# Kernel optimization log

Hardware: AMD Instinct MI355X
Metric: run time of the kernel (lower is better)

Reference implementation:

```python
import jax, jax.numpy as jnp
import numpy as np

DIM = 320
HEADS = 8
D_HEAD = 40
CTX_DIM = 768
INNER_FF = 4 * DIM  # 1280
EPS = 1e-5


def _ln(x, w, b):
    mu = jnp.mean(x, axis=-1, keepdims=True)
    var = jnp.mean(jnp.square(x - mu), axis=-1, keepdims=True)
    return (x - mu) * jax.lax.rsqrt(var + EPS) * w + b


def _attn(xq, ctx, Wq, Wk, Wv, Wo, bo):
    # Wq: [dim, inner]; Wk/Wv: [ctx_dim, inner]; Wo: [inner, dim]
    b, n, _ = xq.shape
    m = ctx.shape[1]
    scale = D_HEAD ** -0.5
    q = (xq @ Wq).reshape(b, n, HEADS, D_HEAD)
    k = (ctx @ Wk).reshape(b, m, HEADS, D_HEAD)
    v = (ctx @ Wv).reshape(b, m, HEADS, D_HEAD)
    sim = jnp.einsum('bihd,bjhd->bhij', q, k) * scale
    attn = jax.nn.softmax(sim, axis=-1)
    out = jnp.einsum('bhij,bjhd->bihd', attn, v).reshape(b, n, HEADS * D_HEAD)
    return out @ Wo + bo


def setup_inputs() -> dict:
    key = jax.random.key(0)
    ks = jax.random.split(key, 20)
    s = 0.02
    inner = HEADS * D_HEAD  # 320
    d = {
        'x': jax.random.normal(ks[0], (2, 4096, DIM), jnp.float32),
        'context': jax.random.normal(ks[1], (2, 77, CTX_DIM), jnp.float32),
        # norm params
        'ln1_w': jnp.ones((DIM,)), 'ln1_b': jnp.zeros((DIM,)),
        'ln2_w': jnp.ones((DIM,)), 'ln2_b': jnp.zeros((DIM,)),
        'ln3_w': jnp.ones((DIM,)), 'ln3_b': jnp.zeros((DIM,)),
        # attn1 (self)
        'a1_Wq': jax.random.normal(ks[2], (DIM, inner)) * s,
        'a1_Wk': jax.random.normal(ks[3], (DIM, inner)) * s,
        'a1_Wv': jax.random.normal(ks[4], (DIM, inner)) * s,
        'a1_Wo': jax.random.normal(ks[5], (inner, DIM)) * s,
        'a1_bo': jnp.zeros((DIM,)),
        # attn2 (cross)
        'a2_Wq': jax.random.normal(ks[6], (DIM, inner)) * s,
        'a2_Wk': jax.random.normal(ks[7], (CTX_DIM, inner)) * s,
        'a2_Wv': jax.random.normal(ks[8], (CTX_DIM, inner)) * s,
        'a2_Wo': jax.random.normal(ks[9], (inner, DIM)) * s,
        'a2_bo': jnp.zeros((DIM,)),
        # GEGLU feed-forward
        'ff_W1': jax.random.normal(ks[10], (DIM, 2 * INNER_FF)) * s,
        'ff_b1': jnp.zeros((2 * INNER_FF,)),
        'ff_W2': jax.random.normal(ks[11], (INNER_FF, DIM)) * s,
        'ff_b2': jnp.zeros((DIM,)),
    }
    return d


def reference(x, context, ln1_w, ln1_b, ln2_w, ln2_b, ln3_w, ln3_b,
              a1_Wq, a1_Wk, a1_Wv, a1_Wo, a1_bo,
              a2_Wq, a2_Wk, a2_Wv, a2_Wo, a2_bo,
              ff_W1, ff_b1, ff_W2, ff_b2):
    h = _ln(x, ln1_w, ln1_b)
    x = _attn(h, h, a1_Wq, a1_Wk, a1_Wv, a1_Wo, a1_bo) + x
    h = _ln(x, ln2_w, ln2_b)
    x = _attn(h, context, a2_Wq, a2_Wk, a2_Wv, a2_Wo, a2_bo) + x
    h = _ln(x, ln3_w, ln3_b)
    proj = h @ ff_W1 + ff_b1
    u, gate = jnp.split(proj, 2, axis=-1)
    ff = (u * jax.nn.gelu(gate, approximate=False)) @ ff_W2 + ff_b2
    return ff + x
```

## Files before the change

kernel.cpp:

```cpp
#include <hip/hip_runtime.h>
#include <hip/hip_bf16.h>
#include <math.h>

typedef __hip_bfloat16 bf16;
typedef __attribute__((ext_vector_type(8))) short bf16x8;
typedef __attribute__((ext_vector_type(4))) short bf16x4;
typedef __attribute__((ext_vector_type(4))) float f32x4;
typedef __attribute__((ext_vector_type(2))) unsigned int u32x2;

#define DIM 320
#define HEADS 8
#define DHEAD 40
#define CTXD 768
#define FFI 1280
#define NQ 4096
#define NCTX 77
#define BATCH 2

static __device__ __forceinline__ short f2bs(float v) {
    union { bf16 b; short s; } x; x.b = __float2bfloat16(v); return x.s;
}
static __device__ __forceinline__ float bs2f(short s) {
    return __uint_as_float(((unsigned)(unsigned short)s) << 16);
}
static __device__ __forceinline__ unsigned pkbf(float hi, float lo) {
    return __builtin_amdgcn_perm(__float_as_uint(hi), __float_as_uint(lo), 0x07060302u);
}

__global__ void __launch_bounds__(256) prep_kernel(
    const float* q1s, const float* k1s, const float* v1s, const float* o1s,
    const float* q2s, const float* o2s, const float* k2s, const float* v2s,
    const float* w1s, const float* w2s,
    short* q1d, short* k1d, short* v1d, short* o1d,
    short* q2d, short* o2d, short* k2d, short* v2d,
    short* w1d, short* w2d,
    const float* x, const float* ln1w, const float* ln1b, short* h)
{
    int bid = blockIdx.x;
    if (bid < 2280) {
        const float* W; short* Wt; int K, N, base;
        if (bid < 600) {
            int ws = bid / 100; base = bid % 100; K = DIM; N = DIM;
            W  = ws == 0 ? q1s : ws == 1 ? k1s : ws == 2 ? v1s : ws == 3 ? o1s : ws == 4 ? q2s : o2s;
            Wt = ws == 0 ? q1d : ws == 1 ? k1d : ws == 2 ? v1d : ws == 3 ? o1d : ws == 4 ? q2d : o2d;
        } else if (bid < 1080) {
            int i = bid - 600; int ws = i / 240; base = i % 240; K = CTXD; N = DIM;
            W = ws ? v2s : k2s; Wt = ws ? v2d : k2d;
        } else if (bid < 1880) {
            base = bid - 1080; K = DIM; N = 2 * FFI; W = w1s; Wt = w1d;
        } else {
            base = bid - 1880; K = FFI; N = DIM; W = w2s; Wt = w2d;
        }
        int ntx = N / 32;
        int n0 = (base % ntx) * 32, k0 = (base / ntx) * 32;
        __shared__ float T[32][33];
        int c = threadIdx.x & 31, r8 = threadIdx.x >> 5;
#pragma unroll
        for (int rr = 0; rr < 4; ++rr) {
            int r = r8 + rr * 8;
            T[r][c] = W[(size_t)(k0 + r) * N + n0 + c];
        }
        __syncthreads();
#pragma unroll
        for (int rr = 0; rr < 4; ++rr) {
            int r = r8 + rr * 8;
            Wt[(size_t)(n0 + r) * K + k0 + c] = f2bs(T[c][r]);
        }
    } else {
        int row = (bid - 2280) * 4 + (threadIdx.x >> 6);
        int lane = threadIdx.x & 63;
        float v[8];
        float s = 0.f, s2 = 0.f;
        if (lane < 40) {
            const float* rp = x + (size_t)row * DIM + lane * 8;
#pragma unroll
            for (int j = 0; j < 8; ++j) { v[j] = rp[j]; s += v[j]; s2 += v[j] * v[j]; }
        }
#pragma unroll
        for (int off = 32; off; off >>= 1) { s += __shfl_xor(s, off); s2 += __shfl_xor(s2, off); }
        float mean = s * (1.f / DIM);
        float var = s2 * (1.f / DIM) - mean * mean;
        float rstd = rsqrtf(var + 1e-5f);
        if (lane < 40) {
            bf16x8 ov;
#pragma unroll
            for (int j = 0; j < 8; ++j)
                ov[j] = f2bs((v[j] - mean) * rstd * ln1w[lane * 8 + j] + ln1b[lane * 8 + j]);
            *(bf16x8*)(h + (size_t)row * DIM + lane * 8) = ov;
        }
    }
}

__global__ void __launch_bounds__(256) ln_b16(const short* __restrict__ srcp,
                          const float* __restrict__ w, const float* __restrict__ bp,
                          short* __restrict__ out)
{
    int row = blockIdx.x * 4 + (threadIdx.x >> 6);
    int lane = threadIdx.x & 63;
    float v[8];
    float s = 0.f, s2 = 0.f;
    if (lane < 40) {
        bf16x8 xv = *(const bf16x8*)(srcp + (size_t)row * DIM + lane * 8);
#pragma unroll
        for (int j = 0; j < 8; ++j) { v[j] = bs2f(xv[j]); s += v[j]; s2 += v[j] * v[j]; }
    }
#pragma unroll
    for (int off = 32; off; off >>= 1) { s += __shfl_xor(s, off); s2 += __shfl_xor(s2, off); }
    float mean = s * (1.f / DIM);
    float var = s2 * (1.f / DIM) - mean * mean;
    float rstd = rsqrtf(var + 1e-5f);
    if (lane < 40) {
        bf16x8 ov;
#pragma unroll
        for (int j = 0; j < 8; ++j)
            ov[j] = f2bs((v[j] - mean) * rstd * w[lane * 8 + j] + bp[lane * 8 + j]);
        *(bf16x8*)(out + (size_t)row * DIM + lane * 8) = ov;
    }
}

template<int MODE>
__global__ void __launch_bounds__(256) gemm128(const short* __restrict__ A,
                          const short* __restrict__ Wt,
                          const float* __restrict__ bias,
                          const float* __restrict__ res,
                          short* __restrict__ resb,
                          short* __restrict__ outb,
                          float* __restrict__ outf,
                          int N, int K, float oscale)
{
    __shared__ short As[128 * 72];
    __shared__ short Bs[64 * 72];
    const int tid = threadIdx.x;
    const int w = tid >> 6, lane = tid & 63, lrow = lane & 15, lgrp = lane >> 4;
    const int wr = w >> 1, wc = w & 1;
    const int m0 = blockIdx.y * 128, n0 = blockIdx.x * 64;
    f32x4 acc[4][2] = {};
    for (int k0 = 0; k0 < K; k0 += 64) {
        __syncthreads();
#pragma unroll
        for (int l = 0; l < 4; ++l) {
            int idx = tid + (l << 8);
            int arow = idx >> 3, ac = idx & 7;
            *(bf16x8*)&As[arow * 72 + ac * 8] =
                *(const bf16x8*)(A + (size_t)(m0 + arow) * K + k0 + ac * 8);
        }
#pragma unroll
        for (int l = 0; l < 2; ++l) {
            int idx = tid + (l << 8);
            int brow = idx >> 3, bc = idx & 7;
            *(bf16x8*)&Bs[brow * 72 + bc * 8] =
                *(const bf16x8*)(Wt + (size_t)(n0 + brow) * K + k0 + bc * 8);
        }
        __syncthreads();
#pragma unroll
        for (int s = 0; s < 2; ++s) {
            bf16x8 b0 = *(const bf16x8*)&Bs[(wc * 32 + lrow) * 72 + s * 32 + lgrp * 8];
            bf16x8 b1 = *(const bf16x8*)&Bs[(wc * 32 + 16 + lrow) * 72 + s * 32 + lgrp * 8];
#pragma unroll
            for (int m = 0; m < 4; ++m) {
                bf16x8 a = *(const bf16x8*)&As[(wr * 64 + m * 16 + lrow) * 72 + s * 32 + lgrp * 8];
                acc[m][0] = __builtin_amdgcn_mfma_f32_16x16x32_bf16(a, b0, acc[m][0], 0, 0, 0);
                acc[m][1] = __builtin_amdgcn_mfma_f32_16x16x32_bf16(a, b1, acc[m][1], 0, 0, 0);
            }
        }
    }
#pragma unroll
    for (int n = 0; n < 2; ++n) {
        int col = n0 + wc * 32 + n * 16 + lrow;
        float bvx = bias ? bias[col] : 0.f;
#pragma unroll
        for (int m = 0; m < 4; ++m) {
#pragma unroll
            for (int r = 0; r < 4; ++r) {
                int row = m0 + wr * 64 + m * 16 + lgrp * 4 + r;
                float v = acc[m][n][r] + bvx;
                size_t o = (size_t)row * N + col;
                if (MODE == 0)      outb[o] = f2bs(v * oscale);
                else if (MODE == 1) resb[o] = f2bs(v + res[o]);
                else if (MODE == 2) resb[o] = f2bs(v + bs2f(resb[o]));
                else                outf[o] = v + bs2f(resb[o]);
            }
        }
    }
}

__global__ void __launch_bounds__(256) qkv128(const short* __restrict__ A,
                          const short* __restrict__ wq, const short* __restrict__ wk,
                          const short* __restrict__ wv,
                          short* __restrict__ qb, short* __restrict__ kbuf,
                          short* __restrict__ vts, float qscale)
{
    __shared__ short As[128 * 72];
    __shared__ short Bs[64 * 72];
    const int tid = threadIdx.x;
    const int z = blockIdx.z;
    const short* Wt = z == 0 ? wq : z == 1 ? wk : wv;
    const int w = tid >> 6, lane = tid & 63, lrow = lane & 15, lgrp = lane >> 4;
    const int wr = w >> 1, wc = w & 1;
    const int m0 = blockIdx.y * 128, n0 = blockIdx.x * 64;
    f32x4 acc[4][2] = {};
    for (int k0 = 0; k0 < DIM; k0 += 64) {
        __syncthreads();
#pragma unroll
        for (int l = 0; l < 4; ++l) {
            int idx = tid + (l << 8);
            int arow = idx >> 3, ac = idx & 7;
            *(bf16x8*)&As[arow * 72 + ac * 8] =
                *(const bf16x8*)(A + (size_t)(m0 + arow) * DIM + k0 + ac * 8);
        }
#pragma unroll
        for (int l = 0; l < 2; ++l) {
            int idx = tid + (l << 8);
            int brow = idx >> 3, bc = idx & 7;
            *(bf16x8*)&Bs[brow * 72 + bc * 8] =
                *(const bf16x8*)(Wt + (size_t)(n0 + brow) * DIM + k0 + bc * 8);
        }
        __syncthreads();
#pragma unroll
        for (int s = 0; s < 2; ++s) {
            bf16x8 b0 = *(const bf16x8*)&Bs[(wc * 32 + lrow) * 72 + s * 32 + lgrp * 8];
            bf16x8 b1 = *(const bf16x8*)&Bs[(wc * 32 + 16 + lrow) * 72 + s * 32 + lgrp * 8];
#pragma unroll
            for (int m = 0; m < 4; ++m) {
                bf16x8 a = *(const bf16x8*)&As[(wr * 64 + m * 16 + lrow) * 72 + s * 32 + lgrp * 8];
                acc[m][0] = __builtin_amdgcn_mfma_f32_16x16x32_bf16(a, b0, acc[m][0], 0, 0, 0);
                acc[m][1] = __builtin_amdgcn_mfma_f32_16x16x32_bf16(a, b1, acc[m][1], 0, 0, 0);
            }
        }
    }
#pragma unroll
    for (int n = 0; n < 2; ++n) {
        int col = n0 + wc * 32 + n * 16 + lrow;
#pragma unroll
        for (int m = 0; m < 4; ++m) {
            if (z == 2) {
                int row0 = m0 + wr * 64 + m * 16 + lgrp * 4;
                int b_ = row0 >> 12, kv = row0 & (NQ - 1);
                int hh = col / DHEAD, d = col - hh * DHEAD;
                bf16x4 pv;
#pragma unroll
                for (int r = 0; r < 4; ++r) pv[r] = f2bs(acc[m][n][r]);
                *(bf16x4*)(vts + (size_t)((b_ * HEADS + hh) * 48 + d) * NQ + kv) = pv;
            } else {
#pragma unroll
                for (int r = 0; r < 4; ++r) {
                    int row = m0 + wr * 64 + m * 16 + lgrp * 4 + r;
                    float v = acc[m][n][r];
                    if (z == 0) qb[(size_t)row * DIM + col] = f2bs(v * qscale);
                    else        kbuf[(size_t)row * DIM + col] = f2bs(v);
                }
            }
        }
    }
}

__global__ void __launch_bounds__(256) crossq_kv(const short* __restrict__ h,
                          const short* __restrict__ wq2,
                          const float* __restrict__ ctx,
                          const short* __restrict__ wk2, const short* __restrict__ wv2,
                          short* __restrict__ qb, short* __restrict__ k2,
                          short* __restrict__ vt2, float qscale)
{
    __shared__ short As[128 * 72];
    __shared__ short Bs[64 * 72];
    const int tid = threadIdx.x;
    const int w = tid >> 6, lane = tid & 63, lrow = lane & 15, lgrp = lane >> 4;
    int bid = blockIdx.x;
    if (bid < 320) {
        const int wr = w >> 1, wc = w & 1;
        const int m0 = (bid / 5) * 128, n0 = (bid % 5) * 64;
        f32x4 acc[4][2] = {};
        for (int k0 = 0; k0 < DIM; k0 += 64) {
            __syncthreads();
#pragma unroll
            for (int l = 0; l < 4; ++l) {
                int idx = tid + (l << 8);
                int arow = idx >> 3, ac = idx & 7;
                *(bf16x8*)&As[arow * 72 + ac * 8] =
                    *(const bf16x8*)(h + (size_t)(m0 + arow) * DIM + k0 + ac * 8);
            }
#pragma unroll
            for (int l = 0; l < 2; ++l) {
                int idx = tid + (l << 8);
                int brow = idx >> 3, bc = idx & 7;
                *(bf16x8*)&Bs[brow * 72 + bc * 8] =
                    *(const bf16x8*)(wq2 + (size_t)(n0 + brow) * DIM + k0 + bc * 8);
            }
            __syncthreads();
#pragma unroll
            for (int s = 0; s < 2; ++s) {
                bf16x8 b0 = *(const bf16x8*)&Bs[(wc * 32 + lrow) * 72 + s * 32 + lgrp * 8];
                bf16x8 b1 = *(const bf16x8*)&Bs[(wc * 32 + 16 + lrow) * 72 + s * 32 + lgrp * 8];
#pragma unroll
                for (int m = 0; m < 4; ++m) {
                    bf16x8 a = *(const bf16x8*)&As[(wr * 64 + m * 16 + lrow) * 72 + s * 32 + lgrp * 8];
                    acc[m][0] = __builtin_amdgcn_mfma_f32_16x16x32_bf16(a, b0, acc[m][0], 0, 0, 0);
                    acc[m][1] = __builtin_amdgcn_mfma_f32_16x16x32_bf16(a, b1, acc[m][1], 0, 0, 0);
                }
            }
        }
#pragma unroll
        for (int n = 0; n < 2; ++n) {
            int col = n0 + wc * 32 + n * 16 + lrow;
#pragma unroll
            for (int m = 0; m < 4; ++m)
#pragma unroll
                for (int r = 0; r < 4; ++r) {
                    int row = m0 + wr * 64 + m * 16 + lgrp * 4 + r;
                    qb[(size_t)row * DIM + col] = f2bs(acc[m][n][r] * qscale);
                }
        }
    } else {
        int i = bid - 320;
        int z = i / 15, r_ = i % 15;
        const short* Wt = z ? wv2 : wk2;
        const int Mc = BATCH * NCTX;
        const int m0 = (r_ / 5) * 64, n0 = (r_ % 5) * 64;
        f32x4 acc[4] = {};
        for (int kb = 0; kb < CTXD / 64; ++kb) {
            const int k0 = kb << 6;
            __syncthreads();
#pragma unroll
            for (int l = 0; l < 2; ++l) {
                int idx = tid + (l << 8);
                int arow = idx >> 3, ac = idx & 7;
                int grow = m0 + arow;
                bf16x8 v = {};
                if (grow < Mc) {
                    const float* Af = ctx + (size_t)grow * CTXD + k0 + ac * 8;
#pragma unroll
                    for (int j = 0; j < 8; ++j) v[j] = f2bs(Af[j]);
                }
                *(bf16x8*)&As[arow * 72 + ac * 8] = v;
                *(bf16x8*)&Bs[arow * 72 + ac * 8] =
                    *(const bf16x8*)(Wt + (size_t)(n0 + arow) * CTXD + k0 + ac * 8);
            }
            __syncthreads();
#pragma unroll
            for (int s = 0; s < 2; ++s) {
                bf16x8 a = *(const bf16x8*)&As[(w * 16 + lrow) * 72 + s * 32 + lgrp * 8];
#pragma unroll
                for (int ct = 0; ct < 4; ++ct) {
                    bf16x8 b = *(const bf16x8*)&Bs[(ct * 16 + lrow) * 72 + s * 32 + lgrp * 8];
                    acc[ct] = __builtin_amdgcn_mfma_f32_16x16x32_bf16(a, b, acc[ct], 0, 0, 0);
                }
            }
        }
#pragma unroll
        for (int ct = 0; ct < 4; ++ct) {
            int col = n0 + ct * 16 + lrow;
            int hh = col / DHEAD, d = col - hh * DHEAD;
#pragma unroll
            for (int r = 0; r < 4; ++r) {
                int row = m0 + w * 16 + lgrp * 4 + r;
                if (row >= Mc) continue;
                float v = acc[ct][r];
                if (z == 0) k2[(size_t)row * DIM + col] = f2bs(v);
                else {
                    int b_ = row / NCTX, kv = row - b_ * NCTX;
                    vt2[(size_t)((b_ * HEADS + hh) * 48 + d) * 128 + kv] = f2bs(v);
                }
            }
        }
    }
}

__global__ void __launch_bounds__(256) geglu128(const short* __restrict__ A,
                           const short* __restrict__ Wt1,
                           const float* __restrict__ b1, short* __restrict__ G)
{
    __shared__ short As[128 * 72];
    __shared__ short Bu[64 * 72];
    __shared__ short Bg[64 * 72];
    const int tid = threadIdx.x;
    const int w = tid >> 6, lane = tid & 63, lrow = lane & 15, lgrp = lane >> 4;
    const int wr = w >> 1, wc = w & 1;
    const int m0 = blockIdx.y * 128, n0 = blockIdx.x * 64;
    f32x4 au[4][2] = {}, ag[4][2] = {};
    for (int k0 = 0; k0 < DIM; k0 += 64) {
        __syncthreads();
#pragma unroll
        for (int l = 0; l < 4; ++l) {
            int idx = tid + (l << 8);
            int arow = idx >> 3, ac = idx & 7;
            *(bf16x8*)&As[arow * 72 + ac * 8] =
                *(const bf16x8*)(A + (size_t)(m0 + arow) * DIM + k0 + ac * 8);
        }
#pragma unroll
        for (int l = 0; l < 2; ++l) {
            int idx = tid + (l << 8);
            int brow = idx >> 3, bc = idx & 7;
            *(bf16x8*)&Bu[brow * 72 + bc * 8] =
                *(const bf16x8*)(Wt1 + (size_t)(n0 + brow) * DIM + k0 + bc * 8);
            *(bf16x8*)&Bg[brow * 72 + bc * 8] =
                *(const bf16x8*)(Wt1 + (size_t)(FFI + n0 + brow) * DIM + k0 + bc * 8);
        }
        __syncthreads();
#pragma unroll
        for (int s = 0; s < 2; ++s) {
            bf16x8 bu0 = *(const bf16x8*)&Bu[(wc * 32 + lrow) * 72 + s * 32 + lgrp * 8];
            bf16x8 bu1 = *(const bf16x8*)&Bu[(wc * 32 + 16 + lrow) * 72 + s * 32 + lgrp * 8];
            bf16x8 bg0 = *(const bf16x8*)&Bg[(wc * 32 + lrow) * 72 + s * 32 + lgrp * 8];
            bf16x8 bg1 = *(const bf16x8*)&Bg[(wc * 32 + 16 + lrow) * 72 + s * 32 + lgrp * 8];
#pragma unroll
            for (int m = 0; m < 4; ++m) {
                bf16x8 a = *(const bf16x8*)&As[(wr * 64 + m * 16 + lrow) * 72 + s * 32 + lgrp * 8];
                au[m][0] = __builtin_amdgcn_mfma_f32_16x16x32_bf16(a, bu0, au[m][0], 0, 0, 0);
                au[m][1] = __builtin_amdgcn_mfma_f32_16x16x32_bf16(a, bu1, au[m][1], 0, 0, 0);
                ag[m][0] = __builtin_amdgcn_mfma_f32_16x16x32_bf16(a, bg0, ag[m][0], 0, 0, 0);
                ag[m][1] = __builtin_amdgcn_mfma_f32_16x16x32_bf16(a, bg1, ag[m][1], 0, 0, 0);
            }
        }
    }
#pragma unroll
    for (int n = 0; n < 2; ++n) {
        int col = n0 + wc * 32 + n * 16 + lrow;
        float bu = b1[col], bg = b1[FFI + col];
#pragma unroll
        for (int m = 0; m < 4; ++m) {
#pragma unroll
            for (int r = 0; r < 4; ++r) {
                int row = m0 + wr * 64 + m * 16 + lgrp * 4 + r;
                float u = au[m][n][r] + bu;
                float g = ag[m][n][r] + bg;
                float gelu = 0.5f * g * (1.f + erff(g * 0.70710678f));
                G[(size_t)row * FFI + col] = f2bs(u * gelu);
            }
        }
    }
}

template<bool FULL>
__global__ void __launch_bounds__(256) flash_mfma(const short* __restrict__ Q,
                           const short* __restrict__ Kb,
                           const short* __restrict__ VtG,
                           short* __restrict__ O,
                           int kvlen, int kvs)
{
    __shared__ short Ks[2][64 * 64];
    __shared__ short Vt[3][48 * 64];
    __shared__ short Ps[128 * 64];
    const int tid = threadIdx.x;
    const int w = tid >> 6, lane = tid & 63, lrow = lane & 15, lgrp = lane >> 4;
    const int hh = blockIdx.y, b = blockIdx.z;
    const int q0 = blockIdx.x * 128;
    const int swz = (lrow & 7) << 4;

    for (int i = tid; i < 1024; i += 256) ((bf16x8*)Ks)[i] = (bf16x8){};
    for (int i = tid; i < 1152; i += 256) {
        short fill = (((i % 384) >> 3) == 40) ? (short)0x3F80 : (short)0;
        bf16x8 f8 = {fill, fill, fill, fill, fill, fill, fill, fill};
        ((bf16x8*)Vt)[i] = f8;
    }

    const size_t qra = (size_t)(b * NQ + q0 + w * 32 + lrow) * DIM + hh * DHEAD;
    const size_t qrb = qra + (size_t)16 * DIM;
    bf16x8 bq0a = *(const bf16x8*)(Q + qra + lgrp * 8);
    bf16x8 bq0b = *(const bf16x8*)(Q + qrb + lgrp * 8);
    bf16x8 bq1a = {}, bq1b = {};
    if (lgrp == 0) {
        bq1a = *(const bf16x8*)(Q + qra + 32);
        bq1b = *(const bf16x8*)(Q + qrb + 32);
    }

    const int kv0 = tid / 5, cc0 = tid % 5;
    const bool isK1 = tid < 64;
    const int kv1 = (256 + tid) / 5, cc1 = (256 + tid) % 5;
    const int vd1 = (tid - 64) >> 3, vcc1 = (tid - 64) & 7;
    const bool hasV2 = tid < 128;
    const int vd2 = (192 + tid) >> 3, vcc2 = (192 + tid) & 7;

    const size_t kbase = (size_t)b * kvlen;
    const size_t vbase = (size_t)((b * HEADS + hh) * 48);

    const short* kp0 = Kb + (kbase + kv0) * DIM + hh * DHEAD + cc0 * 8;
    const short* kp1 = Kb + (kbase + (isK1 ? kv1 : 0)) * DIM + hh * DHEAD + (isK1 ? cc1 : 0) * 8;
    const short* vp1 = VtG + (vbase + (isK1 ? 0 : vd1)) * kvs + (isK1 ? 0 : vcc1) * 8;
    const short* vp2 = VtG + (vbase + (hasV2 ? vd2 : 0)) * kvs + (hasV2 ? vcc2 : 0) * 8;

    const int koff0 = kv0 * 128 + ((cc0 * 16) ^ ((kv0 & 7) << 4));
    const int koff1 = kv1 * 128 + ((cc1 * 16) ^ ((kv1 & 7) << 4));
    const int voff1 = vd1 * 128 + ((vcc1 * 16) ^ ((vd1 & 7) << 4));
    const int voff2 = vd2 * 128 + ((vcc2 * 16) ^ ((vd2 & 7) << 4));

    bf16x8 st0, st1, st2;
    auto issue = [&]() {
        st0 = *(const bf16x8*)kp0; kp0 += 64 * DIM;
        if (isK1) { st1 = *(const bf16x8*)kp1; kp1 += 64 * DIM; }
        else      { st1 = *(const bf16x8*)vp1; vp1 += 64; }
        if (hasV2) { st2 = *(const bf16x8*)vp2; vp2 += 64; }
    };
    auto commit = [&](char* kb_, char* vb_) {
        *(bf16x8*)(kb_ + koff0) = st0;
        if (isK1)  *(bf16x8*)(kb_ + koff1) = st1;
        else       *(bf16x8*)(vb_ + voff1) = st1;
        if (hasV2) *(bf16x8*)(vb_ + voff2) = st2;
    };

    f32x4 oa[3] = {}, ob[3] = {};

    char* kcur = (char*)Ks[0];
    char* knxt = (char*)Ks[1];
    char* vprev = (char*)Vt[2];
    char* vcur  = (char*)Vt[0];
    char* vnxt  = (char*)Vt[1];
    char* pp = (char*)Ps + (w * 32 + lrow) * 128;

    auto pv_step = [&](char* vb_) {
        __builtin_amdgcn_s_setprio(1);
#pragma unroll
        for (int s = 0; s < 2; ++s) {
            bf16x8 bpa = *(const bf16x8*)(pp + ((s * 64 + lgrp * 16) ^ swz));
            bf16x8 bpb = *(const bf16x8*)(pp + 2048 + ((s * 64 + lgrp * 16) ^ swz));
#pragma unroll
            for (int dt = 0; dt < 3; ++dt) {
                bf16x8 av = *(const bf16x8*)(vb_ + (dt * 16 + lrow) * 128 + ((s * 64 + lgrp * 16) ^ swz));
                oa[dt] = __builtin_amdgcn_mfma_f32_16x16x32_bf16(av, bpa, oa[dt], 0, 0, 0);
                ob[dt] = __builtin_amdgcn_mfma_f32_16x16x32_bf16(av, bpb, ob[dt], 0, 0, 0);
            }
        }
        __builtin_amdgcn_s_setprio(0);
    };

    issue();
    __syncthreads();
    commit(kcur, vcur);
    issue();

    const int ntiles = (kvlen + 63) >> 6;
    for (int t = 0; t < ntiles; ++t) {
        __syncthreads();
        commit(knxt, vnxt);
        issue();

        if (t > 0) pv_step(vprev);

        f32x4 sa[4] = {}, sb[4] = {};
        __builtin_amdgcn_s_setprio(1);
#pragma unroll
        for (int ct = 0; ct < 4; ++ct) {
            const char* krow = kcur + (ct * 16 + lrow) * 128;
            bf16x8 ak0 = *(const bf16x8*)(krow + ((lgrp * 16) ^ swz));
            bf16x8 ak1 = *(const bf16x8*)(krow + ((64 + lgrp * 16) ^ swz));
            sa[ct] = __builtin_amdgcn_mfma_f32_16x16x32_bf16(ak0, bq0a, sa[ct], 0, 0, 0);
            sb[ct] = __builtin_amdgcn_mfma_f32_16x16x32_bf16(ak0, bq0b, sb[ct], 0, 0, 0);
            sa[ct] = __builtin_amdgcn_mfma_f32_16x16x32_bf16(ak1, bq1a, sa[ct], 0, 0, 0);
            sb[ct] = __builtin_amdgcn_mfma_f32_16x16x32_bf16(ak1, bq1b, sb[ct], 0, 0, 0);
        }
        __builtin_amdgcn_s_setprio(0);
        if (!FULL && (t << 6) + 64 > kvlen) {
#pragma unroll
            for (int ct = 0; ct < 4; ++ct)
#pragma unroll
                for (int r = 0; r < 4; ++r)
                    if ((t << 6) + ct * 16 + lgrp * 4 + r >= kvlen) { sa[ct][r] = -1e30f; sb[ct][r] = -1e30f; }
        }
#pragma unroll
        for (int ct = 0; ct < 4; ++ct) {
            float a0 = __builtin_amdgcn_exp2f(sa[ct][0]);
            float a1 = __builtin_amdgcn_exp2f(sa[ct][1]);
            float a2 = __builtin_amdgcn_exp2f(sa[ct][2]);
            float a3 = __builtin_amdgcn_exp2f(sa[ct][3]);
            u32x2 pka; pka[0] = pkbf(a1, a0); pka[1] = pkbf(a3, a2);
            *(u32x2*)(pp + ((ct * 32 + lgrp * 8) ^ swz)) = pka;
            float b0 = __builtin_amdgcn_exp2f(sb[ct][0]);
            float b1 = __builtin_amdgcn_exp2f(sb[ct][1]);
            float b2 = __builtin_amdgcn_exp2f(sb[ct][2]);
            float b3 = __builtin_amdgcn_exp2f(sb[ct][3]);
            u32x2 pkb; pkb[0] = pkbf(b1, b0); pkb[1] = pkbf(b3, b2);
            *(u32x2*)(pp + 2048 + ((ct * 32 + lgrp * 8) ^ swz)) = pkb;
        }
        { char* tk = kcur; kcur = knxt; knxt = tk; }
        { char* tv = vprev; vprev = vcur; vcur = vnxt; vnxt = tv; }
    }
    pv_step(vprev);

    float la = __shfl(oa[2][0], 32 + lrow);
    float lb = __shfl(ob[2][0], 32 + lrow);
    float ia = 1.f / la, ib = 1.f / lb;
#pragma unroll
    for (int dt = 0; dt < 3; ++dt) {
        int dbase = dt * 16 + lgrp * 4;
        if (dbase < DHEAD) {
            u32x2 ova, ovb;
            ova[0] = pkbf(oa[dt][1] * ia, oa[dt][0] * ia);
            ova[1] = pkbf(oa[dt][3] * ia, oa[dt][2] * ia);
            *(u32x2*)(O + qra + dbase) = ova;
            ovb[0] = pkbf(ob[dt][1] * ib, ob[dt][0] * ib);
            ovb[1] = pkbf(ob[dt][3] * ib, ob[dt][2] * ib);
            *(u32x2*)(O + qrb + dbase) = ovb;
        }
    }
}

extern "C" void kernel_launch(void* const* d_in, const int* in_sizes, int n_in,
                              void* d_out, int out_size, void* d_ws, size_t ws_size,
                              hipStream_t stream)
{
    const float* x      = (const float*)d_in[0];
    const float* ctx    = (const float*)d_in[1];
    const float* ln1_w  = (const float*)d_in[2];
    const float* ln1_b  = (const float*)d_in[3];
    const float* ln2_w  = (const float*)d_in[4];
    const float* ln2_b  = (const float*)d_in[5];
    const float* ln3_w  = (const float*)d_in[6];
    const float* ln3_b  = (const float*)d_in[7];
    const float* a1_Wq  = (const float*)d_in[8];
    const float* a1_Wk  = (const float*)d_in[9];
    const float* a1_Wv  = (const float*)d_in[10];
    const float* a1_Wo  = (const float*)d_in[11];
    const float* a1_bo  = (const float*)d_in[12];
    const float* a2_Wq  = (const float*)d_in[13];
    const float* a2_Wk  = (const float*)d_in[14];
    const float* a2_Wv  = (const float*)d_in[15];
    const float* a2_Wo  = (const float*)d_in[16];
    const float* a2_bo  = (const float*)d_in[17];
    const float* ff_W1  = (const float*)d_in[18];
    const float* ff_b1  = (const float*)d_in[19];
    const float* ff_W2  = (const float*)d_in[20];
    const float* ff_b2  = (const float*)d_in[21];

    const int M = BATCH * NQ;
    const float qscale2 = (float)(0.15811388300841898 * 1.4426950408889634);

    char* p = (char*)d_ws;
    auto carve = [&](size_t bytes) { char* r = p; p += (bytes + 255) & ~255ULL; return r; };
    short* h       = (short*)carve((size_t)M * DIM * 2);
    short* qb      = (short*)carve((size_t)M * DIM * 2);
    short* kbuf    = (short*)carve((size_t)M * DIM * 2);
    short* attnout = (short*)carve((size_t)M * DIM * 2);
    short* resb    = (short*)carve((size_t)M * DIM * 2);
    short* gbuf    = (short*)carve((size_t)M * FFI * 2);
    short* VtS     = (short*)carve((size_t)BATCH * HEADS * 48 * NQ * 2);
    short* Vt2     = (short*)carve((size_t)BATCH * HEADS * 48 * 128 * 2);
    short* k2      = (short*)carve((size_t)512 * DIM * 2);
    short* wtq1    = (short*)carve((size_t)DIM * DIM * 2);
    short* wtk1    = (short*)carve((size_t)DIM * DIM * 2);
    short* wtv1    = (short*)carve((size_t)DIM * DIM * 2);
    short* wto1    = (short*)carve((size_t)DIM * DIM * 2);
    short* wtq2    = (short*)carve((size_t)DIM * DIM * 2);
    short* wto2    = (short*)carve((size_t)DIM * DIM * 2);
    short* wtk2    = (short*)carve((size_t)DIM * CTXD * 2);
    short* wtv2    = (short*)carve((size_t)DIM * CTXD * 2);
    short* wt1     = (short*)carve((size_t)2 * FFI * DIM * 2);
    short* wt2     = (short*)carve((size_t)DIM * FFI * 2);

    dim3 blk(256);
    dim3 g128(DIM / 64, M / 128);
    dim3 gattn(NQ / 128, HEADS, BATCH);

    prep_kernel<<<2280 + M / 4, blk, 0, stream>>>(
        a1_Wq, a1_Wk, a1_Wv, a1_Wo, a2_Wq, a2_Wo, a2_Wk, a2_Wv, ff_W1, ff_W2,
        wtq1, wtk1, wtv1, wto1, wtq2, wto2, wtk2, wtv2, wt1, wt2,
        x, ln1_w, ln1_b, h);
    qkv128<<<dim3(5, 64, 3), blk, 0, stream>>>(h, wtq1, wtk1, wtv1, qb, kbuf, VtS, qscale2);
    flash_mfma<true><<<gattn, blk, 0, stream>>>(qb, kbuf, VtS, attnout, NQ, NQ);
    gemm128<1><<<g128, blk, 0, stream>>>(attnout, wto1, a1_bo, x, resb, nullptr, nullptr, DIM, DIM, 1.f);
    ln_b16<<<M / 4, blk, 0, stream>>>(resb, ln2_w, ln2_b, h);
    crossq_kv<<<350, blk, 0, stream>>>(h, wtq2, ctx, wtk2, wtv2, qb, k2, Vt2, qscale2);
    flash_mfma<false><<<gattn, blk, 0, stream>>>(qb, k2, Vt2, attnout, NCTX, 128);
    gemm128<2><<<g128, blk, 0, stream>>>(attnout, wto2, a2_bo, nullptr, resb, nullptr, nullptr, DIM, DIM, 1.f);
    ln_b16<<<M / 4, blk, 0, stream>>>(resb, ln3_w, ln3_b, h);
    geglu128<<<dim3(FFI / 64, M / 128), blk, 0, stream>>>(h, wt1, ff_b1, gbuf);
    gemm128<3><<<g128, blk, 0, stream>>>(gbuf, wt2, ff_b2, nullptr, resb, nullptr, (float*)d_out, DIM, FFI, 1.f);
}
```

Baseline: 221.1 us.

## Split self-attention KV range in two and merge partial outputs

The self-attention flash kernel now splits the 4096-key range into two halves. This doubles the grid to 1024 blocks so the GPU's CUs get more concurrent work and better latency hiding. Each half writes unnormalized bf16 partial outputs plus its row sums, and a new combine kernel adds the two partials and normalizes. In exchange it adds an extra launch, extra global traffic for the partial buffers, and a slight precision risk from storing unnormalized sums in bf16. The merge is only valid because the kernel appears to use no per-split running max.

```diff
diff --git a/kernel.cpp b/kernel.cpp
--- a/kernel.cpp
+++ b/kernel.cpp
@@ -118,6 +118,26 @@
     }
 }
 
+__global__ void __launch_bounds__(256) combine_attn(const short* __restrict__ Opart,
+                          const float* __restrict__ lp, short* __restrict__ out)
+{
+    int row = blockIdx.x * 4 + (threadIdx.x >> 6);
+    int lane = threadIdx.x & 63;
+    if (lane >= 40) return;
+    int c = lane * 8;
+    int hh = c / DHEAD;
+    int b_ = row >> 12, q = row & (NQ - 1);
+    float l = lp[((size_t)(0 * 2 + b_) * HEADS + hh) * NQ + q]
+            + lp[((size_t)(1 * 2 + b_) * HEADS + hh) * NQ + q];
+    float inv = 1.f / l;
+    bf16x8 o1 = *(const bf16x8*)(Opart + (size_t)row * DIM + c);
+    bf16x8 o2 = *(const bf16x8*)(Opart + (size_t)(BATCH * NQ) * DIM + (size_t)row * DIM + c);
+    bf16x8 ov;
+#pragma unroll
+    for (int j = 0; j < 8; ++j) ov[j] = f2bs((bs2f(o1[j]) + bs2f(o2[j])) * inv);
+    *(bf16x8*)(out + (size_t)row * DIM + c) = ov;
+}
+
 template<int MODE>
 __global__ void __launch_bounds__(256) gemm128(const short* __restrict__ A,
                           const short* __restrict__ Wt,
@@ -430,19 +450,24 @@
     }
 }
 
-template<bool FULL>
+template<bool SPLIT>
 __global__ void __launch_bounds__(256) flash_mfma(const short* __restrict__ Q,
                            const short* __restrict__ Kb,
                            const short* __restrict__ VtG,
                            short* __restrict__ O,
-                           int kvlen, int kvs)
+                           float* __restrict__ lp,
+                           int kvlen, int kvs, int ntiles)
 {
     __shared__ short Ks[2][64 * 64];
     __shared__ short Vt[3][48 * 64];
     __shared__ short Ps[128 * 64];
     const int tid = threadIdx.x;
     const int w = tid >> 6, lane = tid & 63, lrow = lane & 15, lgrp = lane >> 4;
-    const int hh = blockIdx.y, b = blockIdx.z;
+    const int hh = blockIdx.y;
+    const int zb = blockIdx.z;
+    const int b = SPLIT ? (zb >> 1) : zb;
+    const int hf = SPLIT ? (zb & 1) : 0;
+    const int kvoff = hf * 2048;
     const int q0 = blockIdx.x * 128;
     const int swz = (lrow & 7) << 4;
 
@@ -470,13 +495,13 @@
     const bool hasV2 = tid < 128;
     const int vd2 = (192 + tid) >> 3, vcc2 = (192 + tid) & 7;
 
-    const size_t kbase = (size_t)b * kvlen;
+    const size_t kbase = (size_t)b * kvlen + kvoff;
     const size_t vbase = (size_t)((b * HEADS + hh) * 48);
 
     const short* kp0 = Kb + (kbase + kv0) * DIM + hh * DHEAD + cc0 * 8;
     const short* kp1 = Kb + (kbase + (isK1 ? kv1 : 0)) * DIM + hh * DHEAD + (isK1 ? cc1 : 0) * 8;
-    const short* vp1 = VtG + (vbase + (isK1 ? 0 : vd1)) * kvs + (isK1 ? 0 : vcc1) * 8;
-    const short* vp2 = VtG + (vbase + (hasV2 ? vd2 : 0)) * kvs + (hasV2 ? vcc2 : 0) * 8;
+    const short* vp1 = VtG + (vbase + (isK1 ? 0 : vd1)) * kvs + kvoff + (isK1 ? 0 : vcc1) * 8;
+    const short* vp2 = VtG + (vbase + (hasV2 ? vd2 : 0)) * kvs + kvoff + (hasV2 ? vcc2 : 0) * 8;
 
     const int koff0 = kv0 * 128 + ((cc0 * 16) ^ ((kv0 & 7) << 4));
     const int koff1 = kv1 * 128 + ((cc1 * 16) ^ ((kv1 & 7) << 4));
@@ -527,7 +552,6 @@
     commit(kcur, vcur);
     issue();
 
-    const int ntiles = (kvlen + 63) >> 6;
     for (int t = 0; t < ntiles; ++t) {
         __syncthreads();
         commit(knxt, vnxt);
@@ -548,7 +572,7 @@
             sb[ct] = __builtin_amdgcn_mfma_f32_16x16x32_bf16(ak1, bq1b, sb[ct], 0, 0, 0);
         }
         __builtin_amdgcn_s_setprio(0);
-        if (!FULL && (t << 6) + 64 > kvlen) {
+        if (!SPLIT && (t << 6) + 64 > kvlen) {
 #pragma unroll
             for (int ct = 0; ct < 4; ++ct)
 #pragma unroll
@@ -575,20 +599,42 @@
     }
     pv_step(vprev);
 
-    float la = __shfl(oa[2][0], 32 + lrow);
-    float lb = __shfl(ob[2][0], 32 + lrow);
-    float ia = 1.f / la, ib = 1.f / lb;
-#pragma unroll
-    for (int dt = 0; dt < 3; ++dt) {
-        int dbase = dt * 16 + lgrp * 4;
-        if (dbase < DHEAD) {
-            u32x2 ova, ovb;
-            ova[0] = pkbf(oa[dt][1] * ia, oa[dt][0] * ia);
-            ova[1] = pkbf(oa[dt][3] * ia, oa[dt][2] * ia);
-            *(u32x2*)(O + qra + dbase) = ova;
-            ovb[0] = pkbf(ob[dt][1] * ib, ob[dt][0] * ib);
-            ovb[1] = pkbf(ob[dt][3] * ib, ob[dt][2] * ib);
-            *(u32x2*)(O + qrb + dbase) = ovb;
+    if (SPLIT) {
+        if (lgrp == 2) {
+            size_t lb = ((size_t)(hf * BATCH + b) * HEADS + hh) * NQ + q0 + w * 32;
+            lp[lb + lrow] = oa[2][0];
+            lp[lb + 16 + lrow] = ob[2][0];
+        }
+        const size_t obase = (size_t)hf * BATCH * NQ * DIM;
+#pragma unroll
+        for (int dt = 0; dt < 3; ++dt) {
+            int dbase = dt * 16 + lgrp * 4;
+            if (dbase < DHEAD) {
+                u32x2 ova, ovb;
+                ova[0] = pkbf(oa[dt][1], oa[dt][0]);
+                ova[1] = pkbf(oa[dt][3], oa[dt][2]);
+                *(u32x2*)(O + obase + qra + dbase) = ova;
+                ovb[0] = pkbf(ob[dt][1], ob[dt][0]);
+                ovb[1] = pkbf(ob[dt][3], ob[dt][2]);
+                *(u32x2*)(O + obase + qrb + dbase) = ovb;
+            }
+        }
+    } else {
+        float la = __shfl(oa[2][0], 32 + lrow);
+        float lb2 = __shfl(ob[2][0], 32 + lrow);
+        float ia = 1.f / la, ib = 1.f / lb2;
+#pragma unroll
+        for (int dt = 0; dt < 3; ++dt) {
+            int dbase = dt * 16 + lgrp * 4;
+            if (dbase < DHEAD) {
+                u32x2 ova, ovb;
+                ova[0] = pkbf(oa[dt][1] * ia, oa[dt][0] * ia);
+                ova[1] = pkbf(oa[dt][3] * ia, oa[dt][2] * ia);
+                *(u32x2*)(O + qra + dbase) = ova;
+                ovb[0] = pkbf(ob[dt][1] * ib, ob[dt][0] * ib);
+                ovb[1] = pkbf(ob[dt][3] * ib, ob[dt][2] * ib);
+                *(u32x2*)(O + qrb + dbase) = ovb;
+            }
         }
     }
 }
@@ -634,6 +680,8 @@
     short* VtS     = (short*)carve((size_t)BATCH * HEADS * 48 * NQ * 2);
     short* Vt2     = (short*)carve((size_t)BATCH * HEADS * 48 * 128 * 2);
     short* k2      = (short*)carve((size_t)512 * DIM * 2);
+    short* Opart   = (short*)carve((size_t)2 * M * DIM * 2);
+    float* lp      = (float*)carve((size_t)2 * BATCH * HEADS * NQ * 4);
     short* wtq1    = (short*)carve((size_t)DIM * DIM * 2);
     short* wtk1    = (short*)carve((size_t)DIM * DIM * 2);
     short* wtv1    = (short*)carve((size_t)DIM * DIM * 2);
@@ -647,18 +695,20 @@
 
     dim3 blk(256);
     dim3 g128(DIM / 64, M / 128);
-    dim3 gattn(NQ / 128, HEADS, BATCH);
+    dim3 gattn_s(NQ / 128, HEADS, BATCH * 2);
+    dim3 gattn_c(NQ / 128, HEADS, BATCH);
 
     prep_kernel<<<2280 + M / 4, blk, 0, stream>>>(
         a1_Wq, a1_Wk, a1_Wv, a1_Wo, a2_Wq, a2_Wo, a2_Wk, a2_Wv, ff_W1, ff_W2,
         wtq1, wtk1, wtv1, wto1, wtq2, wto2, wtk2, wtv2, wt1, wt2,
         x, ln1_w, ln1_b, h);
     qkv128<<<dim3(5, 64, 3), blk, 0, stream>>>(h, wtq1, wtk1, wtv1, qb, kbuf, VtS, qscale2);
-    flash_mfma<true><<<gattn, blk, 0, stream>>>(qb, kbuf, VtS, attnout, NQ, NQ);
+    flash_mfma<true><<<gattn_s, blk, 0, stream>>>(qb, kbuf, VtS, Opart, lp, NQ, NQ, 32);
+    combine_attn<<<M / 4, blk, 0, stream>>>(Opart, lp, attnout);
     gemm128<1><<<g128, blk, 0, stream>>>(attnout, wto1, a1_bo, x, resb, nullptr, nullptr, DIM, DIM, 1.f);
     ln_b16<<<M / 4, blk, 0, stream>>>(resb, ln2_w, ln2_b, h);
     crossq_kv<<<350, blk, 0, stream>>>(h, wtq2, ctx, wtk2, wtv2, qb, k2, Vt2, qscale2);
-    flash_mfma<false><<<gattn, blk, 0, stream>>>(qb, k2, Vt2, attnout, NCTX, 128);
+    flash_mfma<false><<<gattn_c, blk, 0, stream>>>(qb, k2, Vt2, attnout, nullptr, NCTX, 128, 2);
     gemm128<2><<<g128, blk, 0, stream>>>(attnout, wto2, a2_bo, nullptr, resb, nullptr, nullptr, DIM, DIM, 1.f);
     ln_b16<<<M / 4, blk, 0, stream>>>(resb, ln3_w, ln3_b, h);
     geglu128<<<dim3(FFI / 64, M / 128), blk, 0, stream>>>(h, wt1, ff_b1, gbuf);
```

After: 230.6 us. 1.04x slower.
